# Kernel optimization log

Measured on AMD Instinct MI355X. Metric: run time of the kernel, lower is better.

## Reference

```python
import jax, jax.numpy as jnp
import numpy as np

NEG_SLOPE = 0.2
NUM_GRAPHS = 64


def _gatv2_layer(x, src, dst, Wl, bl, Wr, br, att, bias, n_nodes, heads, ch):
    # lin_l (source) and lin_r (target) transforms -> [N, H, C]
    xs = (x @ Wl + bl).reshape(n_nodes, heads, ch)
    xd = (x @ Wr + br).reshape(n_nodes, heads, ch)
    s = xs[src]                                   # [E, H, C] gathered source feats
    e = jax.nn.leaky_relu(s + xd[dst], NEG_SLOPE)  # GATv2: leaky_relu BEFORE att dot
    score = jnp.einsum('ehc,hc->eh', e, att)       # [E, H]
    # segment softmax over edges sharing the same target node
    smax = jax.ops.segment_max(score, dst, num_segments=n_nodes)
    ex = jnp.exp(score - smax[dst])
    denom = jax.ops.segment_sum(ex, dst, num_segments=n_nodes)
    alpha = ex / denom[dst]                        # [E, H]
    out = jax.ops.segment_sum(alpha[:, :, None] * s, dst, num_segments=n_nodes)
    return out.reshape(n_nodes, heads * ch) + bias


def setup_inputs() -> dict:
    key = jax.random.key(0)
    ks = jax.random.split(key, 20)
    N, E, F = 50000, 800000, 128
    H, C = 4, 64
    G = NUM_GRAPHS
    sc = 0.05
    inp = {
        'x': jax.random.normal(ks[0], (N, F), jnp.float32),
        'edge_index': jax.random.randint(ks[1], (2, E), 0, N, jnp.int64 if jax.config.read('jax_enable_x64') else jnp.int32).astype(jnp.int32),
        'batch': jnp.sort(jax.random.randint(ks[2], (N,), 0, G)).astype(jnp.int32),
        'W_l1': jax.random.normal(ks[3], (F, H * C)) * sc,
        'b_l1': jax.random.normal(ks[4], (H * C,)) * sc,
        'W_r1': jax.random.normal(ks[5], (F, H * C)) * sc,
        'b_r1': jax.random.normal(ks[6], (H * C,)) * sc,
        'att1': jax.random.normal(ks[7], (H, C)) * sc,
        'bias1': jax.random.normal(ks[8], (H * C,)) * sc,
        'W_l2': jax.random.normal(ks[9], (H * C, C)) * sc,
        'b_l2': jax.random.normal(ks[10], (C,)) * sc,
        'W_r2': jax.random.normal(ks[11], (H * C, C)) * sc,
        'b_r2': jax.random.normal(ks[12], (C,)) * sc,
        'att2': jax.random.normal(ks[13], (1, C)) * sc,
        'bias2': jax.random.normal(ks[14], (C,)) * sc,
        'W_lin': jax.random.normal(ks[15], (C, 1)) * sc,
        'b_lin': jax.random.normal(ks[16], (1,)) * sc,
    }
    return inp


def reference(x, edge_index, batch, W_l1, b_l1, W_r1, b_r1, att1, bias1,
              W_l2, b_l2, W_r2, b_r2, att2, bias2, W_lin, b_lin):
    N = x.shape[0]
    # PyG GATv2Conv adds self-loops by default
    loops = jnp.arange(N, dtype=edge_index.dtype)
    src = jnp.concatenate([edge_index[0], loops])
    dst = jnp.concatenate([edge_index[1], loops])

    h = _gatv2_layer(x, src, dst, W_l1, b_l1, W_r1, b_r1, att1, bias1, N, 4, 64)
    h = jax.nn.relu(h)  # dropout=identity (eval), norm=Identity
    h = _gatv2_layer(h, src, dst, W_l2, b_l2, W_r2, b_r2, att2, bias2, N, 1, 64)

    # global mean pool over graphs
    sums = jax.ops.segment_sum(h, batch, num_segments=NUM_GRAPHS)
    counts = jax.ops.segment_sum(jnp.ones((N,), h.dtype), batch, num_segments=NUM_GRAPHS)
    pooled = sums / jnp.maximum(counts, 1.0)[:, None]  # [G, 64]
    return pooled @ W_lin + b_lin                      # [G, 1]
```

## Files before the change

### kernel.cpp

```cpp
#include <hip/hip_runtime.h>
#include <hip/hip_bf16.h>
#include <math.h>

typedef __attribute__((ext_vector_type(8))) short short8;
typedef __attribute__((ext_vector_type(4))) float floatx4;

__device__ __forceinline__ float bf2f(unsigned short u) {
  union { unsigned int i; float f; } v; v.i = ((unsigned int)u) << 16; return v.f;
}
__device__ __forceinline__ unsigned short f2bf(float f) {
  union { float f; unsigned int u; } v; v.f = f;
  unsigned int r = (v.u + 0x7fffu + ((v.u >> 16) & 1u)) >> 16;
  return (unsigned short)r;
}
__device__ __forceinline__ int imin(int a, int b) { return a < b ? a : b; }
__device__ __forceinline__ int iclamp(int v, int lo, int hi) {
  return v < lo ? lo : (v > hi ? hi : v);
}
__device__ __forceinline__ float uasf(unsigned int u) {
  union { unsigned int i; float f; } v; v.i = u; return v.f;
}
__device__ __forceinline__ float sum16(float x) {
  union { float f; int i; } a, t;
  a.f = x;
  t.i = __builtin_amdgcn_update_dpp(0, a.i, 0x121, 0xF, 0xF, true); a.f += t.f;
  t.i = __builtin_amdgcn_update_dpp(0, a.i, 0x122, 0xF, 0xF, true); a.f += t.f;
  t.i = __builtin_amdgcn_update_dpp(0, a.i, 0x124, 0xF, 0xF, true); a.f += t.f;
  t.i = __builtin_amdgcn_update_dpp(0, a.i, 0x128, 0xF, 0xF, true); a.f += t.f;
  return a.f;
}

__global__ void k_sentinel(float* out, float val) {
  if (threadIdx.x < 64) out[threadIdx.x] = val;
}

struct CvtSegs {
  const void* src[10];
  unsigned short* dst[10];
  int len[10];
};

__global__ void k_prep(const void* __restrict__ x, unsigned short* __restrict__ x_c,
                       int n8, CvtSegs segs,
                       const void* __restrict__ s0, const void* __restrict__ s1,
                       const void* __restrict__ s2, const void* __restrict__ s3,
                       unsigned short* __restrict__ d0, unsigned short* __restrict__ d1,
                       unsigned short* __restrict__ d2, unsigned short* __restrict__ d3,
                       const int* __restrict__ edst, int* deg, int E, int N,
                       int* dflag, int* colx, int ET, int nCvt8, int nTransB) {
  __shared__ int csh;
  if (threadIdx.x == 0) csh = 0;
  __syncthreads();
  {
    unsigned short u = ((const unsigned short*)x)[threadIdx.x];
    int e = (u >> 7) & 0xFF;
    atomicAdd(&csh, (u == 0) || (e >= 100 && e <= 145));
  }
  __syncthreads();
  int isf = (csh < 240);

  int b = blockIdx.x;
  if (b < nCvt8) {
    if (!isf) return;
    int i = b * 256 + threadIdx.x;
    if (i >= n8) return;
    const float* s = (const float*)x + (size_t)i * 8;
    ushort4 a, c;
    a.x = f2bf(s[0]); a.y = f2bf(s[1]); a.z = f2bf(s[2]); a.w = f2bf(s[3]);
    c.x = f2bf(s[4]); c.y = f2bf(s[5]); c.z = f2bf(s[6]); c.w = f2bf(s[7]);
    ((ushort4*)x_c)[i * 2] = a;
    ((ushort4*)x_c)[i * 2 + 1] = c;
    return;
  }
  b -= nCvt8;
  if (b < 10) {
    if (b == 0) {
      if (threadIdx.x == 0) dflag[0] = isf;
      if (threadIdx.x >= 248) colx[ET + (threadIdx.x - 248)] = 0;
    }
    int i = threadIdx.x;
    if (i < segs.len[b])
      segs.dst[b][i] = isf ? f2bf(((const float*)segs.src[b])[i])
                           : ((const unsigned short*)segs.src[b])[i];
    return;
  }
  b -= 10;
  if (b < nTransB) {
    int idx = b * 256 + threadIdx.x;
    const void* src; unsigned short* dst; int R, C, loc;
    if (idx < 32768)      { src = s0; dst = d0; R = 128; C = 256; loc = idx; }
    else if (idx < 65536) { src = s1; dst = d1; R = 128; C = 256; loc = idx - 32768; }
    else if (idx < 81920) { src = s2; dst = d2; R = 256; C = 64;  loc = idx - 65536; }
    else                  { src = s3; dst = d3; R = 256; C = 64;  loc = idx - 81920; }
    unsigned short u = isf ? f2bf(((const float*)src)[loc])
                           : ((const unsigned short*)src)[loc];
    int r = loc / C, cc = loc - r * C;
    dst[cc * R + r] = u;
    return;
  }
  b -= nTransB;
  int e = b * 256 + threadIdx.x;
  if (e < E) atomicAdd(&deg[iclamp(edst[e], 0, N - 1)], 1);
}

__global__ __launch_bounds__(1024) void k_scan1(const int* __restrict__ deg, int* bsum, int N) {
  __shared__ int sm[1024];
  int tid = threadIdx.x;
  int i = blockIdx.x * 1024 + tid;
  sm[tid] = (i < N) ? deg[i] + 1 : 0;
  __syncthreads();
  for (int off = 512; off > 0; off >>= 1) {
    if (tid < off) sm[tid] += sm[tid + off];
    __syncthreads();
  }
  if (tid == 0) bsum[blockIdx.x] = sm[0];
}

__global__ __launch_bounds__(1024) void k_scan3(const int* __restrict__ deg,
                                                const int* __restrict__ bsum,
                                                int* rowptr, int* cursor, int N) {
  __shared__ int sm[1024];
  __shared__ int boff;
  int tid = threadIdx.x;
  if (tid == 0) {
    int r = 0;
    for (int b = 0; b < blockIdx.x; ++b) r += bsum[b];
    boff = r;
  }
  int i = blockIdx.x * 1024 + tid;
  int v = (i < N) ? deg[i] + 1 : 0;
  sm[tid] = v;
  __syncthreads();
  for (int off = 1; off < 1024; off <<= 1) {
    int t = (tid >= off) ? sm[tid - off] : 0;
    __syncthreads();
    sm[tid] += t;
    __syncthreads();
  }
  if (i < N) {
    int ex = sm[tid] - v + boff;
    rowptr[i] = ex;
    cursor[i] = ex;
    if (i == N - 1) rowptr[N] = ex + v;
  }
}

template <int K, int CT, int RT>
__device__ __forceinline__ void gemm2r_body(
    int bx, int by, int tid,
    const unsigned short* __restrict__ A,
    const unsigned short* __restrict__ BTl, const unsigned short* __restrict__ BTr,
    const unsigned short* __restrict__ bl, const unsigned short* __restrict__ br,
    unsigned short* __restrict__ outl, unsigned short* __restrict__ outr,
    int Nrows, int M) {
  constexpr int KI = K / 32;
  int lane = tid & 63;
  int wave = tid >> 6;
  int r = lane & 15, q = lane >> 4;
  int col0 = by * (4 * CT * 16) + wave * (CT * 16);
  int row0 = bx * (16 * RT);
  short8 Bl[KI][CT], Br[KI][CT];
#pragma unroll
  for (int t = 0; t < CT; ++t) {
    const unsigned short* bpl = BTl + (size_t)(col0 + t * 16 + r) * K + q * 8;
    const unsigned short* bpr = BTr + (size_t)(col0 + t * 16 + r) * K + q * 8;
#pragma unroll
    for (int k = 0; k < KI; ++k) {
      Bl[k][t] = *reinterpret_cast<const short8*>(bpl + k * 32);
      Br[k][t] = *reinterpret_cast<const short8*>(bpr + k * 32);
    }
  }
  float bvl[CT], bvr[CT];
#pragma unroll
  for (int t = 0; t < CT; ++t) {
    bvl[t] = bf2f(bl[col0 + t * 16 + r]);
    bvr[t] = bf2f(br[col0 + t * 16 + r]);
  }
  short8 a[KI], an[KI];
  {
    int ar0 = imin(row0 + r, Nrows - 1);
    const unsigned short* Ap = A + (size_t)ar0 * K + q * 8;
#pragma unroll
    for (int k = 0; k < KI; ++k) a[k] = *reinterpret_cast<const short8*>(Ap + k * 32);
  }
  for (int rt = 0; rt < RT; ++rt) {
    if (rt + 1 < RT) {
      int arn = imin(row0 + (rt + 1) * 16 + r, Nrows - 1);
      const unsigned short* Apn = A + (size_t)arn * K + q * 8;
#pragma unroll
      for (int k = 0; k < KI; ++k) an[k] = *reinterpret_cast<const short8*>(Apn + k * 32);
    }
    floatx4 accl[CT], accr[CT];
#pragma unroll
    for (int t = 0; t < CT; ++t) {
      accl[t] = (floatx4){0.f, 0.f, 0.f, 0.f};
      accr[t] = (floatx4){0.f, 0.f, 0.f, 0.f};
    }
#pragma unroll
    for (int k = 0; k < KI; ++k) {
#pragma unroll
      for (int t = 0; t < CT; ++t) {
        accl[t] = __builtin_amdgcn_mfma_f32_16x16x32_bf16(a[k], Bl[k][t], accl[t], 0, 0, 0);
        accr[t] = __builtin_amdgcn_mfma_f32_16x16x32_bf16(a[k], Br[k][t], accr[t], 0, 0, 0);
      }
    }
#pragma unroll
    for (int t = 0; t < CT; ++t) {
      int col = col0 + t * 16 + r;
#pragma unroll
      for (int rr = 0; rr < 4; ++rr) {
        int row = row0 + rt * 16 + q * 4 + rr;
        if (row < Nrows) {
          outl[(size_t)row * M + col] = f2bf(accl[t][rr] + bvl[t]);
          outr[(size_t)row * M + col] = f2bf(accr[t][rr] + bvr[t]);
        }
      }
    }
#pragma unroll
    for (int k = 0; k < KI; ++k) a[k] = an[k];
  }
}

__global__ __launch_bounds__(256) void k_phase1(
    const unsigned short* __restrict__ A0, const unsigned short* __restrict__ A1,
    const int* __restrict__ dflag,
    const unsigned short* __restrict__ BTl, const unsigned short* __restrict__ BTr,
    const unsigned short* __restrict__ bl, const unsigned short* __restrict__ br,
    unsigned short* __restrict__ outl, unsigned short* __restrict__ outr,
    int Nrows, int M, int nRB, int nG,
    const int* __restrict__ esrc, const int* __restrict__ edst,
    const int* __restrict__ rowptr, int* cursor, int* colx, int E, int N) {
  int b = blockIdx.x;
  if (b < nG) {
    const unsigned short* A = dflag[0] ? A1 : A0;
    gemm2r_body<128, 2, 8>(b >> 1, b & 1, threadIdx.x, A, BTl, BTr, bl, br,
                           outl, outr, Nrows, M);
    return;
  }
  b -= nG;
  int e = b * 256 + threadIdx.x;
  int ET = E + N;
  if (e < ET) {
    if (e < E) {
      int s = iclamp(esrc[e], 0, N - 1), d = iclamp(edst[e], 0, N - 1);
      int pos = atomicAdd(&cursor[d], 1);
      colx[iclamp(pos, 0, ET - 1)] = s;
    } else {
      int i = e - E;
      colx[rowptr[i + 1] - 1] = i;
    }
  }
}

__global__ __launch_bounds__(256) void k_gemm2r_l2(
    const unsigned short* __restrict__ A,
    const unsigned short* __restrict__ BTl, const unsigned short* __restrict__ BTr,
    const unsigned short* __restrict__ bl, const unsigned short* __restrict__ br,
    unsigned short* __restrict__ outl, unsigned short* __restrict__ outr,
    int Nrows, int M) {
  gemm2r_body<256, 1, 4>(blockIdx.x, 0, threadIdx.x, A, BTl, BTr, bl, br,
                         outl, outr, Nrows, M);
}

#define UNPACK2(u, v0, v1, v2, v3)          \
  v0 = uasf(u.x << 16); v1 = uasf(u.x & 0xffff0000u); \
  v2 = uasf(u.y << 16); v3 = uasf(u.y & 0xffff0000u);

#define SCORE(q0, q1, q2, q3, p)                             \
  p = q0 * 0.6f;                                             \
  p = fmaf(q1, 0.6f, p); p = fmaf(q2, 0.6f, p); p = fmaf(q3, 0.6f, p); \
  p = fmaf(c0, fabsf(q0), p); p = fmaf(c1, fabsf(q1), p);    \
  p = fmaf(c2, fabsf(q2), p); p = fmaf(c3, fabsf(q3), p);

__global__ __launch_bounds__(256) void k_agg_h4(
    const int* __restrict__ rowptr, const int* __restrict__ colx,
    const unsigned short* __restrict__ xs, const unsigned short* __restrict__ xd,
    const unsigned short* __restrict__ att, const unsigned short* __restrict__ bias,
    unsigned short* __restrict__ hout, int N) {
  int lane = threadIdx.x & 63;
  int dst = (blockIdx.x * 256 + threadIdx.x) >> 6;
  if (dst >= N) return;
  int off = lane << 2;
  unsigned int off2 = (unsigned int)off * 2;
  const char* xsb = (const char*)xs;
  ushort4 au = *reinterpret_cast<const ushort4*>(att + off);
  ushort4 du = *reinterpret_cast<const ushort4*>(xd + (size_t)dst * 256 + off);
  float a0 = bf2f(au.x), a1 = bf2f(au.y), a2 = bf2f(au.z), a3 = bf2f(au.w);
  float d0 = bf2f(du.x), d1 = bf2f(du.y), d2 = bf2f(du.z), d3 = bf2f(du.w);
  float ad0 = a0 * d0, ad1 = a1 * d1, ad2 = a2 * d2, ad3 = a3 * d3;
  float c0 = copysignf(0.4f, a0), c1 = copysignf(0.4f, a1);
  float c2 = copysignf(0.4f, a2), c3 = copysignf(0.4f, a3);
  float l = 0.f, o0 = 0.f, o1 = 0.f, o2 = 0.f, o3 = 0.f;
  int beg = __builtin_amdgcn_readfirstlane(rowptr[dst]);
  int end = __builtin_amdgcn_readfirstlane(rowptr[dst + 1]);
  int i0 = colx[beg], i1 = colx[beg + 1];
  int i2 = colx[beg + 2], i3 = colx[beg + 3];
  uint2 ua = *(const uint2*)(xsb + (((unsigned)i0 << 9) + off2));
  uint2 ub = *(const uint2*)(xsb + (((unsigned)i1 << 9) + off2));
  uint2 uc = *(const uint2*)(xsb + (((unsigned)i2 << 9) + off2));
  uint2 ud = *(const uint2*)(xsb + (((unsigned)i3 << 9) + off2));
  for (int e = beg; e < end; e += 4) {
    uint2 na = ua, nb = ub, nc = uc, nd = ud;
    int np = e + 4;
    if (np < end) {
      int t0 = colx[np], t1 = colx[np + 1];
      int t2 = colx[np + 2], t3 = colx[np + 3];
      na = *(const uint2*)(xsb + (((unsigned)t0 << 9) + off2));
      nb = *(const uint2*)(xsb + (((unsigned)t1 << 9) + off2));
      nc = *(const uint2*)(xsb + (((unsigned)t2 << 9) + off2));
      nd = *(const uint2*)(xsb + (((unsigned)t3 << 9) + off2));
    }
    float va0, va1, va2, va3, vb0, vb1, vb2, vb3;
    float vc0, vc1, vc2, vc3, vd0, vd1, vd2, vd3;
    UNPACK2(ua, va0, va1, va2, va3)
    UNPACK2(ub, vb0, vb1, vb2, vb3)
    UNPACK2(uc, vc0, vc1, vc2, vc3)
    UNPACK2(ud, vd0, vd1, vd2, vd3)
    float qa0 = fmaf(a0, va0, ad0), qa1 = fmaf(a1, va1, ad1);
    float qa2 = fmaf(a2, va2, ad2), qa3 = fmaf(a3, va3, ad3);
    float qb0 = fmaf(a0, vb0, ad0), qb1 = fmaf(a1, vb1, ad1);
    float qb2 = fmaf(a2, vb2, ad2), qb3 = fmaf(a3, vb3, ad3);
    float qc0 = fmaf(a0, vc0, ad0), qc1 = fmaf(a1, vc1, ad1);
    float qc2 = fmaf(a2, vc2, ad2), qc3 = fmaf(a3, vc3, ad3);
    float qd0 = fmaf(a0, vd0, ad0), qd1 = fmaf(a1, vd1, ad1);
    float qd2 = fmaf(a2, vd2, ad2), qd3 = fmaf(a3, vd3, ad3);
    float pa, pb, pc, pd;
    SCORE(qa0, qa1, qa2, qa3, pa)
    SCORE(qb0, qb1, qb2, qb3, pb)
    SCORE(qc0, qc1, qc2, qc3, pc)
    SCORE(qd0, qd1, qd2, qd3, pd)
    pa = sum16(pa); pb = sum16(pb); pc = sum16(pc); pd = sum16(pd);
    pa = fminf(fmaxf(pa, -60.f), 60.f);
    pb = (e + 1 < end) ? fminf(fmaxf(pb, -60.f), 60.f) : -INFINITY;
    pc = (e + 2 < end) ? fminf(fmaxf(pc, -60.f), 60.f) : -INFINITY;
    pd = (e + 3 < end) ? fminf(fmaxf(pd, -60.f), 60.f) : -INFINITY;
    float wa = __expf(pa), wb = __expf(pb), wc = __expf(pc), wd = __expf(pd);
    l += (wa + wb) + (wc + wd);
    o0 = fmaf(wa, va0, o0); o0 = fmaf(wb, vb0, o0);
    o0 = fmaf(wc, vc0, o0); o0 = fmaf(wd, vd0, o0);
    o1 = fmaf(wa, va1, o1); o1 = fmaf(wb, vb1, o1);
    o1 = fmaf(wc, vc1, o1); o1 = fmaf(wd, vd1, o1);
    o2 = fmaf(wa, va2, o2); o2 = fmaf(wb, vb2, o2);
    o2 = fmaf(wc, vc2, o2); o2 = fmaf(wd, vd2, o2);
    o3 = fmaf(wa, va3, o3); o3 = fmaf(wb, vb3, o3);
    o3 = fmaf(wc, vc3, o3); o3 = fmaf(wd, vd3, o3);
    ua = na; ub = nb; uc = nc; ud = nd;
  }
  float rl = 1.0f / l;
  ushort4 bu = *reinterpret_cast<const ushort4*>(bias + off);
  ushort4 res;
  res.x = f2bf(fmaxf(fmaf(o0, rl, bf2f(bu.x)), 0.f));
  res.y = f2bf(fmaxf(fmaf(o1, rl, bf2f(bu.y)), 0.f));
  res.z = f2bf(fmaxf(fmaf(o2, rl, bf2f(bu.z)), 0.f));
  res.w = f2bf(fmaxf(fmaf(o3, rl, bf2f(bu.w)), 0.f));
  *reinterpret_cast<ushort4*>(hout + (size_t)dst * 256 + off) = res;
}

__global__ __launch_bounds__(256) void k_agg_h1(
    const int* __restrict__ rowptr, const int* __restrict__ colx,
    const unsigned short* __restrict__ xs, const unsigned short* __restrict__ xd,
    const unsigned short* __restrict__ att, const unsigned short* __restrict__ bias,
    float* __restrict__ hout, int N) {
  int lane = threadIdx.x & 63;
  int wid = (blockIdx.x * 256 + threadIdx.x) >> 6;
  int g = lane >> 4, sl = lane & 15;
  int dst = wid * 4 + g;
  bool valid = dst < N;
  int dsafe = valid ? dst : 0;
  int cb = sl << 2;
  unsigned int cb2 = (unsigned int)cb * 2;
  const char* xsb = (const char*)xs;
  ushort4 au = *reinterpret_cast<const ushort4*>(att + cb);
  ushort4 du = *reinterpret_cast<const ushort4*>(xd + (size_t)dsafe * 64 + cb);
  float a0 = bf2f(au.x), a1 = bf2f(au.y), a2 = bf2f(au.z), a3 = bf2f(au.w);
  float d0 = bf2f(du.x), d1 = bf2f(du.y), d2 = bf2f(du.z), d3 = bf2f(du.w);
  float ad0 = a0 * d0, ad1 = a1 * d1, ad2 = a2 * d2, ad3 = a3 * d3;
  float c0 = copysignf(0.4f, a0), c1 = copysignf(0.4f, a1);
  float c2 = copysignf(0.4f, a2), c3 = copysignf(0.4f, a3);
  float l = 0.f, o0 = 0.f, o1 = 0.f, o2 = 0.f, o3 = 0.f;
  int beg = valid ? rowptr[dst] : 0;
  int end = valid ? rowptr[dst + 1] : 0;
  if (end > beg) {
    int i0 = colx[beg], i1 = colx[beg + 1];
    int i2 = colx[beg + 2], i3 = colx[beg + 3];
    uint2 ua = *(const uint2*)(xsb + (((unsigned)i0 << 7) + cb2));
    uint2 ub = *(const uint2*)(xsb + (((unsigned)i1 << 7) + cb2));
    uint2 uc = *(const uint2*)(xsb + (((unsigned)i2 << 7) + cb2));
    uint2 ud = *(const uint2*)(xsb + (((unsigned)i3 << 7) + cb2));
    for (int e = beg; e < end; e += 4) {
      uint2 na = ua, nb = ub, nc = uc, nd = ud;
      int np = e + 4;
      if (np < end) {
        int t0 = colx[np], t1 = colx[np + 1];
        int t2 = colx[np + 2], t3 = colx[np + 3];
        na = *(const uint2*)(xsb + (((unsigned)t0 << 7) + cb2));
        nb = *(const uint2*)(xsb + (((unsigned)t1 << 7) + cb2));
        nc = *(const uint2*)(xsb + (((unsigned)t2 << 7) + cb2));
        nd = *(const uint2*)(xsb + (((unsigned)t3 << 7) + cb2));
      }
      float va0, va1, va2, va3, vb0, vb1, vb2, vb3;
      float vc0, vc1, vc2, vc3, vd0, vd1, vd2, vd3;
      UNPACK2(ua, va0, va1, va2, va3)
      UNPACK2(ub, vb0, vb1, vb2, vb3)
      UNPACK2(uc, vc0, vc1, vc2, vc3)
      UNPACK2(ud, vd0, vd1, vd2, vd3)
      float qa0 = fmaf(a0, va0, ad0), qa1 = fmaf(a1, va1, ad1);
      float qa2 = fmaf(a2, va2, ad2), qa3 = fmaf(a3, va3, ad3);
      float qb0 = fmaf(a0, vb0, ad0), qb1 = fmaf(a1, vb1, ad1);
      float qb2 = fmaf(a2, vb2, ad2), qb3 = fmaf(a3, vb3, ad3);
      float qc0 = fmaf(a0, vc0, ad0), qc1 = fmaf(a1, vc1, ad1);
      float qc2 = fmaf(a2, vc2, ad2), qc3 = fmaf(a3, vc3, ad3);
      float qd0 = fmaf(a0, vd0, ad0), qd1 = fmaf(a1, vd1, ad1);
      float qd2 = fmaf(a2, vd2, ad2), qd3 = fmaf(a3, vd3, ad3);
      float pa, pb, pc, pd;
      SCORE(qa0, qa1, qa2, qa3, pa)
      SCORE(qb0, qb1, qb2, qb3, pb)
      SCORE(qc0, qc1, qc2, qc3, pc)
      SCORE(qd0, qd1, qd2, qd3, pd)
      pa = sum16(pa); pb = sum16(pb); pc = sum16(pc); pd = sum16(pd);
      pa = fminf(fmaxf(pa, -60.f), 60.f);
      pb = (e + 1 < end) ? fminf(fmaxf(pb, -60.f), 60.f) : -INFINITY;
      pc = (e + 2 < end) ? fminf(fmaxf(pc, -60.f), 60.f) : -INFINITY;
      pd = (e + 3 < end) ? fminf(fmaxf(pd, -60.f), 60.f) : -INFINITY;
      float wa = __expf(pa), wb = __expf(pb), wc = __expf(pc), wd = __expf(pd);
      l += (wa + wb) + (wc + wd);
      o0 = fmaf(wa, va0, o0); o0 = fmaf(wb, vb0, o0);
      o0 = fmaf(wc, vc0, o0); o0 = fmaf(wd, vd0, o0);
      o1 = fmaf(wa, va1, o1); o1 = fmaf(wb, vb1, o1);
      o1 = fmaf(wc, vc1, o1); o1 = fmaf(wd, vd1, o1);
      o2 = fmaf(wa, va2, o2); o2 = fmaf(wb, vb2, o2);
      o2 = fmaf(wc, vc2, o2); o2 = fmaf(wd, vd2, o2);
      o3 = fmaf(wa, va3, o3); o3 = fmaf(wb, vb3, o3);
      o3 = fmaf(wc, vc3, o3); o3 = fmaf(wd, vd3, o3);
      ua = na; ub = nb; uc = nc; ud = nd;
    }
  }
  if (valid) {
    float rl = 1.0f / l;
    ushort4 bu = *reinterpret_cast<const ushort4*>(bias + cb);
    floatx4 res;
    res[0] = fmaf(o0, rl, bf2f(bu.x));
    res[1] = fmaf(o1, rl, bf2f(bu.y));
    res[2] = fmaf(o2, rl, bf2f(bu.z));
    res[3] = fmaf(o3, rl, bf2f(bu.w));
    *reinterpret_cast<floatx4*>(hout + (size_t)dst * 64 + cb) = res;
  }
}

__global__ __launch_bounds__(256) void k_pool(const float* __restrict__ h2,
                                              const int* __restrict__ batch,
                                              float* pool, int* cnt, int N) {
  int lane = threadIdx.x & 63;
  int wid = (blockIdx.x * 256 + threadIdx.x) >> 6;
  int n0 = wid * 32;
  if (n0 >= N) return;
  int nend = imin(n0 + 32, N);
  float acc = 0.f;
  int c = 0;
  int gcur = iclamp(batch[n0], 0, 63);
  for (int n = n0; n < nend; ++n) {
    int gg = iclamp(batch[n], 0, 63);
    if (gg != gcur) {
      atomicAdd(&pool[gcur * 64 + lane], acc);
      if (lane == 0) atomicAdd(&cnt[gcur], c);
      acc = 0.f; c = 0; gcur = gg;
    }
    acc += h2[(size_t)n * 64 + lane];
    c++;
  }
  atomicAdd(&pool[gcur * 64 + lane], acc);
  if (lane == 0) atomicAdd(&cnt[gcur], c);
}

__global__ void k_final(const float* __restrict__ pool, const int* __restrict__ cnt,
                        const unsigned short* __restrict__ Wlinc,
                        const unsigned short* __restrict__ blinc,
                        float* __restrict__ out) {
  int g = threadIdx.x;
  if (g >= 64) return;
  float inv = 1.f / fmaxf((float)cnt[g], 1.f);
  float s = 0.f;
  for (int c = 0; c < 64; ++c) s += pool[g * 64 + c] * bf2f(Wlinc[c]);
  out[g] = fmaf(s, inv, bf2f(blinc[0]));
}

extern "C" void kernel_launch(void* const* d_in, const int* in_sizes, int n_in,
                              void* d_out, int out_size, void* d_ws, size_t ws_size,
                              hipStream_t stream) {
  const void* x     = d_in[0];
  const int*  ei    = (const int*)d_in[1];
  const int*  batch = (const int*)d_in[2];
  const void* Wl1 = d_in[3];  const void* bl1 = d_in[4];
  const void* Wr1 = d_in[5];  const void* br1 = d_in[6];
  const void* att1 = d_in[7]; const void* bias1 = d_in[8];
  const void* Wl2 = d_in[9];  const void* bl2 = d_in[10];
  const void* Wr2 = d_in[11]; const void* br2 = d_in[12];
  const void* att2 = d_in[13]; const void* bias2 = d_in[14];
  const void* Wlin = d_in[15]; const void* blin = d_in[16];
  float* out = (float*)d_out;

  const int F = 128, HC = 256, C2 = 64;
  int N = in_sizes[0] / F;
  int E = in_sizes[1] / 2;
  int ET = E + N;
  const int* esrc = ei;
  const int* edst = ei + E;

  char* w = (char*)d_ws;
  auto alloc = [&](size_t bytes) {
    char* p = w;
    w += (bytes + 255) & ~(size_t)255;
    return p;
  };
  int* dflag  = (int*)alloc(4);
  int* rowptr = (int*)alloc((size_t)(N + 1) * 4);
  int* cursor = (int*)alloc((size_t)N * 4);
  int* bsum   = (int*)alloc(1024 * 4);
  int* colx   = (int*)alloc((size_t)(ET + 8) * 4);
  unsigned short* smallc = (unsigned short*)alloc(4096);
  unsigned short* Wl1T = (unsigned short*)alloc((size_t)F * HC * 2);
  unsigned short* Wr1T = (unsigned short*)alloc((size_t)F * HC * 2);
  unsigned short* Wl2T = (unsigned short*)alloc((size_t)HC * C2 * 2);
  unsigned short* Wr2T = (unsigned short*)alloc((size_t)HC * C2 * 2);
  int* deg    = (int*)alloc((size_t)N * 4);
  float* pool = (float*)alloc(64 * 64 * 4);
  int* cnt    = (int*)alloc(64 * 4);
  unsigned short* xs1  = (unsigned short*)alloc((size_t)N * HC * 2);
  unsigned short* xd1  = (unsigned short*)alloc((size_t)N * HC * 2);
  unsigned short* h1   = (unsigned short*)alloc((size_t)N * HC * 2);
  size_t required = (size_t)(w - (char*)d_ws);
  size_t zlen = (size_t)((char*)cnt + 256 - (char*)deg);

  unsigned short* x_c = h1;
  unsigned short* xs2 = xs1;
  unsigned short* xd2 = xs1 + (size_t)N * C2;
  float*          h2  = (float*)xd1;

  unsigned short* bl1c   = smallc + 0;
  unsigned short* br1c   = smallc + 256;
  unsigned short* att1c  = smallc + 512;
  unsigned short* bias1c = smallc + 768;
  unsigned short* bl2c   = smallc + 1024;
  unsigned short* br2c   = smallc + 1088;
  unsigned short* att2c  = smallc + 1152;
  unsigned short* bias2c = smallc + 1216;
  unsigned short* Wlinc  = smallc + 1280;
  unsigned short* blinc  = smallc + 1344;

  if (ws_size < required) {
    k_sentinel<<<1, 64, 0, stream>>>(out, 1000.f + (float)(ws_size >> 20));
    return;
  }

  hipMemsetAsync(deg, 0, zlen, stream);

  CvtSegs segs;
  const void* ssrc[10] = {bl1, br1, att1, bias1, bl2, br2, att2, bias2, Wlin, blin};
  unsigned short* sdst[10] = {bl1c, br1c, att1c, bias1c, bl2c, br2c, att2c, bias2c, Wlinc, blinc};
  int slen[10] = {256, 256, 256, 256, 64, 64, 64, 64, 64, 1};
  for (int i = 0; i < 10; ++i) { segs.src[i] = ssrc[i]; segs.dst[i] = sdst[i]; segs.len[i] = slen[i]; }
  int n8 = N * F / 8;
  int nCvt8 = (n8 + 255) / 256;
  int nTransB = (2 * F * HC + 2 * HC * C2 + 255) / 256;
  int nHist = (E + 255) / 256;
  k_prep<<<nCvt8 + 10 + nTransB + nHist, 256, 0, stream>>>(
      x, x_c, n8, segs, Wl1, Wr1, Wl2, Wr2, Wl1T, Wr1T, Wl2T, Wr2T,
      edst, deg, E, N, dflag, colx, ET, nCvt8, nTransB);

  int nb = (N + 1023) / 1024;
  k_scan1<<<nb, 1024, 0, stream>>>(deg, bsum, N);
  k_scan3<<<nb, 1024, 0, stream>>>(deg, bsum, rowptr, cursor, N);

  int nRB = (N + 127) / 128;
  int nG = nRB * 2;
  int nS = (ET + 255) / 256;
  k_phase1<<<nG + nS, 256, 0, stream>>>(
      (const unsigned short*)x, x_c, dflag, Wl1T, Wr1T, bl1c, br1c, xs1, xd1,
      N, HC, nRB, nG, esrc, edst, rowptr, cursor, colx, E, N);

  k_agg_h4<<<(N + 3) / 4, 256, 0, stream>>>(rowptr, colx, xs1, xd1, att1c, bias1c, h1, N);

  k_gemm2r_l2<<<(N + 63) / 64, 256, 0, stream>>>(h1, Wl2T, Wr2T, bl2c, br2c, xs2, xd2, N, C2);
  k_agg_h1<<<(N + 15) / 16, 256, 0, stream>>>(rowptr, colx, xs2, xd2, att2c, bias2c, h2, N);

  int pw = (N + 31) / 32;
  k_pool<<<(pw + 3) / 4, 256, 0, stream>>>(h2, batch, pool, cnt, N);
  k_final<<<1, 64, 0, stream>>>(pool, cnt, Wlinc, blinc, out);
}
```

Baseline: 346.9 us.

## Fuse layer-1 GEMM into prep kernel with on-the-fly bf16 conversion

Moves the layer-1 dual GEMM into the prep kernel and converts x and the layer-1 weights from fp32 to bf16 while loading them into MFMA fragments. This removes the separate x conversion pass, the weight transpose and the x_c buffer round trip. The edge scatter moves into its own kernel after the scan, and the degree histogram now handles four edges per thread. The risk is slow strided fp32 weight loads (column-wise, 8 scalar loads per fragment) and per-element conversion inside the GEMM blocks.

```diff
diff --git a/kernel.cpp b/kernel.cpp
--- a/kernel.cpp
+++ b/kernel.cpp
@@ -30,6 +30,29 @@
   return a.f;
 }
 
+__device__ __forceinline__ short8 load_a_frag(const void* A, int row, int K,
+                                              int off, int isf) {
+  if (isf) {
+    const float* p = (const float*)A + (size_t)row * K + off;
+    short8 v;
+#pragma unroll
+    for (int j = 0; j < 8; ++j) v[j] = (short)f2bf(p[j]);
+    return v;
+  }
+  return *reinterpret_cast<const short8*>((const unsigned short*)A + (size_t)row * K + off);
+}
+__device__ __forceinline__ short8 load_b_raw(const void* W, int col, int kbase,
+                                             int M, int isf) {
+  short8 v;
+#pragma unroll
+  for (int j = 0; j < 8; ++j) {
+    int k = kbase + j;
+    v[j] = isf ? (short)f2bf(((const float*)W)[(size_t)k * M + col])
+               : (short)((const unsigned short*)W)[(size_t)k * M + col];
+  }
+  return v;
+}
+
 __global__ void k_sentinel(float* out, float val) {
   if (threadIdx.x < 64) out[threadIdx.x] = val;
 }
@@ -40,14 +63,16 @@
   int len[10];
 };
 
-__global__ void k_prep(const void* __restrict__ x, unsigned short* __restrict__ x_c,
-                       int n8, CvtSegs segs,
-                       const void* __restrict__ s0, const void* __restrict__ s1,
-                       const void* __restrict__ s2, const void* __restrict__ s3,
-                       unsigned short* __restrict__ d0, unsigned short* __restrict__ d1,
-                       unsigned short* __restrict__ d2, unsigned short* __restrict__ d3,
-                       const int* __restrict__ edst, int* deg, int E, int N,
-                       int* dflag, int* colx, int ET, int nCvt8, int nTransB) {
+__global__ __launch_bounds__(256) void k_prep(
+    const void* __restrict__ x, CvtSegs segs,
+    const void* __restrict__ Wl1, const void* __restrict__ Wr1,
+    const void* __restrict__ bl1, const void* __restrict__ br1,
+    const void* __restrict__ s2, const void* __restrict__ s3,
+    unsigned short* __restrict__ d2, unsigned short* __restrict__ d3,
+    const int* __restrict__ edst, int* deg, int E, int N,
+    int* colx, int ET,
+    unsigned short* __restrict__ xs1, unsigned short* __restrict__ xd1,
+    int nHist, int nTransB) {
   __shared__ int csh;
   if (threadIdx.x == 0) csh = 0;
   __syncthreads();
@@ -60,22 +85,18 @@
   int isf = (csh < 240);
 
   int b = blockIdx.x;
-  if (b < nCvt8) {
-    if (!isf) return;
-    int i = b * 256 + threadIdx.x;
-    if (i >= n8) return;
-    const float* s = (const float*)x + (size_t)i * 8;
-    ushort4 a, c;
-    a.x = f2bf(s[0]); a.y = f2bf(s[1]); a.z = f2bf(s[2]); a.w = f2bf(s[3]);
-    c.x = f2bf(s[4]); c.y = f2bf(s[5]); c.z = f2bf(s[6]); c.w = f2bf(s[7]);
-    ((ushort4*)x_c)[i * 2] = a;
-    ((ushort4*)x_c)[i * 2 + 1] = c;
+  if (b < nHist) {
+    int base = b * 1024 + threadIdx.x;
+#pragma unroll
+    for (int k = 0; k < 4; ++k) {
+      int e = base + k * 256;
+      if (e < E) atomicAdd(&deg[iclamp(edst[e], 0, N - 1)], 1);
+    }
     return;
   }
-  b -= nCvt8;
+  b -= nHist;
   if (b < 10) {
     if (b == 0) {
-      if (threadIdx.x == 0) dflag[0] = isf;
       if (threadIdx.x >= 248) colx[ET + (threadIdx.x - 248)] = 0;
     }
     int i = threadIdx.x;
@@ -87,20 +108,82 @@
   b -= 10;
   if (b < nTransB) {
     int idx = b * 256 + threadIdx.x;
-    const void* src; unsigned short* dst; int R, C, loc;
-    if (idx < 32768)      { src = s0; dst = d0; R = 128; C = 256; loc = idx; }
-    else if (idx < 65536) { src = s1; dst = d1; R = 128; C = 256; loc = idx - 32768; }
-    else if (idx < 81920) { src = s2; dst = d2; R = 256; C = 64;  loc = idx - 65536; }
-    else                  { src = s3; dst = d3; R = 256; C = 64;  loc = idx - 81920; }
+    const void* src; unsigned short* dst; int loc;
+    if (idx < 16384) { src = s2; dst = d2; loc = idx; }
+    else             { src = s3; dst = d3; loc = idx - 16384; }
     unsigned short u = isf ? f2bf(((const float*)src)[loc])
                            : ((const unsigned short*)src)[loc];
-    int r = loc / C, cc = loc - r * C;
-    dst[cc * R + r] = u;
+    int r = loc / 64, cc = loc - r * 64;
+    dst[cc * 256 + r] = u;
     return;
   }
   b -= nTransB;
-  int e = b * 256 + threadIdx.x;
-  if (e < E) atomicAdd(&deg[iclamp(edst[e], 0, N - 1)], 1);
+  {
+    int bx = b >> 1, by = b & 1;
+    int lane = threadIdx.x & 63;
+    int wave = threadIdx.x >> 6;
+    int r = lane & 15, q = lane >> 4;
+    int col0 = by * 128 + wave * 32;
+    int row0 = bx * 128;
+    short8 Bl[4][2], Br[4][2];
+#pragma unroll
+    for (int t = 0; t < 2; ++t) {
+      int col = col0 + t * 16 + r;
+#pragma unroll
+      for (int k = 0; k < 4; ++k) {
+        Bl[k][t] = load_b_raw(Wl1, col, k * 32 + q * 8, 256, isf);
+        Br[k][t] = load_b_raw(Wr1, col, k * 32 + q * 8, 256, isf);
+      }
+    }
+    float bvl[2], bvr[2];
+#pragma unroll
+    for (int t = 0; t < 2; ++t) {
+      int col = col0 + t * 16 + r;
+      bvl[t] = isf ? ((const float*)bl1)[col] : bf2f(((const unsigned short*)bl1)[col]);
+      bvr[t] = isf ? ((const float*)br1)[col] : bf2f(((const unsigned short*)br1)[col]);
+    }
+    short8 a[4], an[4];
+    {
+      int ar0 = imin(row0 + r, N - 1);
+#pragma unroll
+      for (int k = 0; k < 4; ++k) a[k] = load_a_frag(x, ar0, 128, k * 32 + q * 8, isf);
+    }
+    for (int rt = 0; rt < 8; ++rt) {
+      if (rt + 1 < 8) {
+        int arn = imin(row0 + (rt + 1) * 16 + r, N - 1);
+#pragma unroll
+        for (int k = 0; k < 4; ++k) an[k] = load_a_frag(x, arn, 128, k * 32 + q * 8, isf);
+      }
+      floatx4 accl[2], accr[2];
+#pragma unroll
+      for (int t = 0; t < 2; ++t) {
+        accl[t] = (floatx4){0.f, 0.f, 0.f, 0.f};
+        accr[t] = (floatx4){0.f, 0.f, 0.f, 0.f};
+      }
+#pragma unroll
+      for (int k = 0; k < 4; ++k) {
+#pragma unroll
+        for (int t = 0; t < 2; ++t) {
+          accl[t] = __builtin_amdgcn_mfma_f32_16x16x32_bf16(a[k], Bl[k][t], accl[t], 0, 0, 0);
+          accr[t] = __builtin_amdgcn_mfma_f32_16x16x32_bf16(a[k], Br[k][t], accr[t], 0, 0, 0);
+        }
+      }
+#pragma unroll
+      for (int t = 0; t < 2; ++t) {
+        int col = col0 + t * 16 + r;
+#pragma unroll
+        for (int rr = 0; rr < 4; ++rr) {
+          int row = row0 + rt * 16 + q * 4 + rr;
+          if (row < N) {
+            xs1[(size_t)row * 256 + col] = f2bf(accl[t][rr] + bvl[t]);
+            xd1[(size_t)row * 256 + col] = f2bf(accr[t][rr] + bvr[t]);
+          }
+        }
+      }
+#pragma unroll
+      for (int k = 0; k < 4; ++k) a[k] = an[k];
+    }
+  }
 }
 
 __global__ __launch_bounds__(1024) void k_scan1(const int* __restrict__ deg, int* bsum, int N) {
@@ -142,6 +225,23 @@
     rowptr[i] = ex;
     cursor[i] = ex;
     if (i == N - 1) rowptr[N] = ex + v;
+  }
+}
+
+__global__ void k_scatter(const int* __restrict__ esrc, const int* __restrict__ edst,
+                          const int* __restrict__ rowptr, int* cursor, int* colx,
+                          int E, int N) {
+  int e = blockIdx.x * 256 + threadIdx.x;
+  int ET = E + N;
+  if (e < ET) {
+    if (e < E) {
+      int s = iclamp(esrc[e], 0, N - 1), d = iclamp(edst[e], 0, N - 1);
+      int pos = atomicAdd(&cursor[d], 1);
+      colx[iclamp(pos, 0, ET - 1)] = s;
+    } else {
+      int i = e - E;
+      colx[rowptr[i + 1] - 1] = i;
+    }
   }
 }
 
@@ -218,37 +318,6 @@
     }
 #pragma unroll
     for (int k = 0; k < KI; ++k) a[k] = an[k];
-  }
-}
-
-__global__ __launch_bounds__(256) void k_phase1(
-    const unsigned short* __restrict__ A0, const unsigned short* __restrict__ A1,
-    const int* __restrict__ dflag,
-    const unsigned short* __restrict__ BTl, const unsigned short* __restrict__ BTr,
-    const unsigned short* __restrict__ bl, const unsigned short* __restrict__ br,
-    unsigned short* __restrict__ outl, unsigned short* __restrict__ outr,
-    int Nrows, int M, int nRB, int nG,
-    const int* __restrict__ esrc, const int* __restrict__ edst,
-    const int* __restrict__ rowptr, int* cursor, int* colx, int E, int N) {
-  int b = blockIdx.x;
-  if (b < nG) {
-    const unsigned short* A = dflag[0] ? A1 : A0;
-    gemm2r_body<128, 2, 8>(b >> 1, b & 1, threadIdx.x, A, BTl, BTr, bl, br,
-                           outl, outr, Nrows, M);
-    return;
-  }
-  b -= nG;
-  int e = b * 256 + threadIdx.x;
-  int ET = E + N;
-  if (e < ET) {
-    if (e < E) {
-      int s = iclamp(esrc[e], 0, N - 1), d = iclamp(edst[e], 0, N - 1);
-      int pos = atomicAdd(&cursor[d], 1);
-      colx[iclamp(pos, 0, ET - 1)] = s;
-    } else {
-      int i = e - E;
-      colx[rowptr[i + 1] - 1] = i;
-    }
   }
 }
 
@@ -512,14 +581,11 @@
     w += (bytes + 255) & ~(size_t)255;
     return p;
   };
-  int* dflag  = (int*)alloc(4);
   int* rowptr = (int*)alloc((size_t)(N + 1) * 4);
   int* cursor = (int*)alloc((size_t)N * 4);
   int* bsum   = (int*)alloc(1024 * 4);
   int* colx   = (int*)alloc((size_t)(ET + 8) * 4);
   unsigned short* smallc = (unsigned short*)alloc(4096);
-  unsigned short* Wl1T = (unsigned short*)alloc((size_t)F * HC * 2);
-  unsigned short* Wr1T = (unsigned short*)alloc((size_t)F * HC * 2);
   unsigned short* Wl2T = (unsigned short*)alloc((size_t)HC * C2 * 2);
   unsigned short* Wr2T = (unsigned short*)alloc((size_t)HC * C2 * 2);
   int* deg    = (int*)alloc((size_t)N * 4);
@@ -531,7 +597,6 @@
   size_t required = (size_t)(w - (char*)d_ws);
   size_t zlen = (size_t)((char*)cnt + 256 - (char*)deg);
 
-  unsigned short* x_c = h1;
   unsigned short* xs2 = xs1;
   unsigned short* xd2 = xs1 + (size_t)N * C2;
   float*          h2  = (float*)xd1;
@@ -559,24 +624,18 @@
   unsigned short* sdst[10] = {bl1c, br1c, att1c, bias1c, bl2c, br2c, att2c, bias2c, Wlinc, blinc};
   int slen[10] = {256, 256, 256, 256, 64, 64, 64, 64, 64, 1};
   for (int i = 0; i < 10; ++i) { segs.src[i] = ssrc[i]; segs.dst[i] = sdst[i]; segs.len[i] = slen[i]; }
-  int n8 = N * F / 8;
-  int nCvt8 = (n8 + 255) / 256;
-  int nTransB = (2 * F * HC + 2 * HC * C2 + 255) / 256;
-  int nHist = (E + 255) / 256;
-  k_prep<<<nCvt8 + 10 + nTransB + nHist, 256, 0, stream>>>(
-      x, x_c, n8, segs, Wl1, Wr1, Wl2, Wr2, Wl1T, Wr1T, Wl2T, Wr2T,
-      edst, deg, E, N, dflag, colx, ET, nCvt8, nTransB);
+  int nHist = (E + 1023) / 1024;
+  int nTransB = (2 * HC * C2 + 255) / 256;
+  int nG = ((N + 127) / 128) * 2;
+  k_prep<<<nHist + 10 + nTransB + nG, 256, 0, stream>>>(
+      x, segs, Wl1, Wr1, bl1, br1, Wl2, Wr2, Wl2T, Wr2T,
+      edst, deg, E, N, colx, ET, xs1, xd1, nHist, nTransB);
 
   int nb = (N + 1023) / 1024;
   k_scan1<<<nb, 1024, 0, stream>>>(deg, bsum, N);
   k_scan3<<<nb, 1024, 0, stream>>>(deg, bsum, rowptr, cursor, N);
 
-  int nRB = (N + 127) / 128;
-  int nG = nRB * 2;
-  int nS = (ET + 255) / 256;
-  k_phase1<<<nG + nS, 256, 0, stream>>>(
-      (const unsigned short*)x, x_c, dflag, Wl1T, Wr1T, bl1c, br1c, xs1, xd1,
-      N, HC, nRB, nG, esrc, edst, rowptr, cursor, colx, E, N);
+  k_scatter<<<(ET + 255) / 256, 256, 0, stream>>>(esrc, edst, rowptr, cursor, colx, E, N);
 
   k_agg_h4<<<(N + 3) / 4, 256, 0, stream>>>(rowptr, colx, xs1, xd1, att1c, bias1c, h1, N);
 
```

After: 419.2 us. 20.8% more time.

## Fuse pooling with final linear and interleave GEMM and CSR scatter blocks

Applied to the files above, without the earlier changes.

Pooling and the final linear layer become one kernel with one block per graph. Each block finds its node range by binary search over the sorted batch array, which removes the global atomics, the pool/count buffers and part of the memset. In the phase-1 kernel, GEMM blocks and edge-scatter blocks are now interleaved across the grid so both kinds of work run together, and each scatter block handles 1024 edges instead of 256. A FMA pair in the aggregation loop is also reordered, which slightly changes floating-point summation order. Risks: pooling parallelism drops to 64 blocks, and the binary search assumes batch is sorted.

```diff
diff --git a/kernel.cpp b/kernel.cpp
--- a/kernel.cpp
+++ b/kernel.cpp
@@ -227,27 +227,35 @@
     const unsigned short* __restrict__ BTl, const unsigned short* __restrict__ BTr,
     const unsigned short* __restrict__ bl, const unsigned short* __restrict__ br,
     unsigned short* __restrict__ outl, unsigned short* __restrict__ outr,
-    int Nrows, int M, int nRB, int nG,
+    int Nrows, int M, int nG, int nS,
     const int* __restrict__ esrc, const int* __restrict__ edst,
     const int* __restrict__ rowptr, int* cursor, int* colx, int E, int N) {
   int b = blockIdx.x;
-  if (b < nG) {
+  int m2 = 2 * imin(nG, nS);
+  bool isG;
+  int idx;
+  if (b < m2) { isG = (b & 1) == 0; idx = b >> 1; }
+  else        { isG = nG > nS;      idx = imin(nG, nS) + (b - m2); }
+  if (isG) {
     const unsigned short* A = dflag[0] ? A1 : A0;
-    gemm2r_body<128, 2, 8>(b >> 1, b & 1, threadIdx.x, A, BTl, BTr, bl, br,
+    gemm2r_body<128, 2, 8>(idx >> 1, idx & 1, threadIdx.x, A, BTl, BTr, bl, br,
                            outl, outr, Nrows, M);
     return;
   }
-  b -= nG;
-  int e = b * 256 + threadIdx.x;
   int ET = E + N;
-  if (e < ET) {
-    if (e < E) {
-      int s = iclamp(esrc[e], 0, N - 1), d = iclamp(edst[e], 0, N - 1);
-      int pos = atomicAdd(&cursor[d], 1);
-      colx[iclamp(pos, 0, ET - 1)] = s;
-    } else {
-      int i = e - E;
-      colx[rowptr[i + 1] - 1] = i;
+  int base = idx * 1024 + threadIdx.x;
+#pragma unroll
+  for (int k = 0; k < 4; ++k) {
+    int e = base + k * 256;
+    if (e < ET) {
+      if (e < E) {
+        int s = iclamp(esrc[e], 0, N - 1), d = iclamp(edst[e], 0, N - 1);
+        int pos = atomicAdd(&cursor[d], 1);
+        colx[iclamp(pos, 0, ET - 1)] = s;
+      } else {
+        int i = e - E;
+        colx[rowptr[i + 1] - 1] = i;
+      }
     }
   }
 }
@@ -431,7 +439,7 @@
       o2 = fmaf(wa, va2, o2); o2 = fmaf(wb, vb2, o2);
       o2 = fmaf(wc, vc2, o2); o2 = fmaf(wd, vd2, o2);
       o3 = fmaf(wa, va3, o3); o3 = fmaf(wb, vb3, o3);
-      o3 = fmaf(wc, vc3, o3); o3 = fmaf(wd, vd3, o3);
+      o3 = fmaf(wd, vd3, o3); o3 = fmaf(wc, vc3, o3);
       ua = na; ub = nb; uc = nc; ud = nd;
     }
   }
@@ -447,41 +455,38 @@
   }
 }
 
-__global__ __launch_bounds__(256) void k_pool(const float* __restrict__ h2,
-                                              const int* __restrict__ batch,
-                                              float* pool, int* cnt, int N) {
-  int lane = threadIdx.x & 63;
-  int wid = (blockIdx.x * 256 + threadIdx.x) >> 6;
-  int n0 = wid * 32;
-  if (n0 >= N) return;
-  int nend = imin(n0 + 32, N);
+__global__ __launch_bounds__(256) void k_poolfinal(
+    const float* __restrict__ h2, const int* __restrict__ batch,
+    const unsigned short* __restrict__ Wlinc, const unsigned short* __restrict__ blinc,
+    float* __restrict__ out, int N) {
+  __shared__ float sm[4][64];
+  __shared__ int bounds[2];
+  int g = blockIdx.x;
+  int tid = threadIdx.x;
+  if (tid < 2) {
+    int target = g + tid;
+    int lo = 0, hi = N;
+    while (lo < hi) {
+      int mid = (lo + hi) >> 1;
+      if (batch[mid] < target) lo = mid + 1; else hi = mid;
+    }
+    bounds[tid] = lo;
+  }
+  __syncthreads();
+  int lo = bounds[0], hi = bounds[1];
+  int lane = tid & 63, wv = tid >> 6;
   float acc = 0.f;
-  int c = 0;
-  int gcur = iclamp(batch[n0], 0, 63);
-  for (int n = n0; n < nend; ++n) {
-    int gg = iclamp(batch[n], 0, 63);
-    if (gg != gcur) {
-      atomicAdd(&pool[gcur * 64 + lane], acc);
-      if (lane == 0) atomicAdd(&cnt[gcur], c);
-      acc = 0.f; c = 0; gcur = gg;
-    }
-    acc += h2[(size_t)n * 64 + lane];
-    c++;
-  }
-  atomicAdd(&pool[gcur * 64 + lane], acc);
-  if (lane == 0) atomicAdd(&cnt[gcur], c);
-}
-
-__global__ void k_final(const float* __restrict__ pool, const int* __restrict__ cnt,
-                        const unsigned short* __restrict__ Wlinc,
-                        const unsigned short* __restrict__ blinc,
-                        float* __restrict__ out) {
-  int g = threadIdx.x;
-  if (g >= 64) return;
-  float inv = 1.f / fmaxf((float)cnt[g], 1.f);
-  float s = 0.f;
-  for (int c = 0; c < 64; ++c) s += pool[g * 64 + c] * bf2f(Wlinc[c]);
-  out[g] = fmaf(s, inv, bf2f(blinc[0]));
+  for (int n = lo + wv; n < hi; n += 4) acc += h2[(size_t)n * 64 + lane];
+  sm[wv][lane] = acc;
+  __syncthreads();
+  if (tid < 64) {
+    float s = sm[0][tid] + sm[1][tid] + sm[2][tid] + sm[3][tid];
+    float inv = 1.f / fmaxf((float)(hi - lo), 1.f);
+    float v = s * inv * bf2f(Wlinc[tid]);
+    v += __shfl_xor(v, 1);  v += __shfl_xor(v, 2);  v += __shfl_xor(v, 4);
+    v += __shfl_xor(v, 8);  v += __shfl_xor(v, 16); v += __shfl_xor(v, 32);
+    if (tid == 0) out[g] = v + bf2f(blinc[0]);
+  }
 }
 
 extern "C" void kernel_launch(void* const* d_in, const int* in_sizes, int n_in,
@@ -523,13 +528,10 @@
   unsigned short* Wl2T = (unsigned short*)alloc((size_t)HC * C2 * 2);
   unsigned short* Wr2T = (unsigned short*)alloc((size_t)HC * C2 * 2);
   int* deg    = (int*)alloc((size_t)N * 4);
-  float* pool = (float*)alloc(64 * 64 * 4);
-  int* cnt    = (int*)alloc(64 * 4);
   unsigned short* xs1  = (unsigned short*)alloc((size_t)N * HC * 2);
   unsigned short* xd1  = (unsigned short*)alloc((size_t)N * HC * 2);
   unsigned short* h1   = (unsigned short*)alloc((size_t)N * HC * 2);
   size_t required = (size_t)(w - (char*)d_ws);
-  size_t zlen = (size_t)((char*)cnt + 256 - (char*)deg);
 
   unsigned short* x_c = h1;
   unsigned short* xs2 = xs1;
@@ -552,7 +554,7 @@
     return;
   }
 
-  hipMemsetAsync(deg, 0, zlen, stream);
+  hipMemsetAsync(deg, 0, (size_t)N * 4, stream);
 
   CvtSegs segs;
   const void* ssrc[10] = {bl1, br1, att1, bias1, bl2, br2, att2, bias2, Wlin, blin};
@@ -571,19 +573,16 @@
   k_scan1<<<nb, 1024, 0, stream>>>(deg, bsum, N);
   k_scan3<<<nb, 1024, 0, stream>>>(deg, bsum, rowptr, cursor, N);
 
-  int nRB = (N + 127) / 128;
-  int nG = nRB * 2;
-  int nS = (ET + 255) / 256;
+  int nG = ((N + 127) / 128) * 2;
+  int nS = (ET + 1023) / 1024;
   k_phase1<<<nG + nS, 256, 0, stream>>>(
       (const unsigned short*)x, x_c, dflag, Wl1T, Wr1T, bl1c, br1c, xs1, xd1,
-      N, HC, nRB, nG, esrc, edst, rowptr, cursor, colx, E, N);
+      N, HC, nG, nS, esrc, edst, rowptr, cursor, colx, E, N);
 
   k_agg_h4<<<(N + 3) / 4, 256, 0, stream>>>(rowptr, colx, xs1, xd1, att1c, bias1c, h1, N);
 
   k_gemm2r_l2<<<(N + 63) / 64, 256, 0, stream>>>(h1, Wl2T, Wr2T, bl2c, br2c, xs2, xd2, N, C2);
   k_agg_h1<<<(N + 15) / 16, 256, 0, stream>>>(rowptr, colx, xs2, xd2, att2c, bias2c, h2, N);
 
-  int pw = (N + 31) / 32;
-  k_pool<<<(pw + 3) / 4, 256, 0, stream>>>(h2, batch, pool, cnt, N);
-  k_final<<<1, 64, 0, stream>>>(pool, cnt, Wlinc, blinc, out);
-}
+  k_poolfinal<<<64, 256, 0, stream>>>(h2, batch, Wlinc, blinc, out, N);
+}
```

After: 366.3 us. 5.6% more time.
